# Performance work log

Measured on AMD Instinct MI355X. Metric: run time of the kernel, lower is better.

Reference implementation:

```python
import jax, jax.numpy as jnp
import numpy as np

B, N, T = 32, 128, 16          # batch, nb_nodes, total algorithm steps (1 no-hint + T-1 hinted)
FN, FE, FG, FH = 16, 8, 8, 16  # raw node/edge/graph/hint feature widths
H, DEC = 128, 64               # hidden_dim, decoder output width
MSG_STEPS = 3                  # msg_passing_steps
NEG = -1e9


def setup_inputs() -> dict:
    key = jax.random.key(0)
    ks = jax.random.split(key, 20)
    def nrm(k, shape, s=0.1):
        return jax.random.normal(k, shape, dtype=jnp.float32) * s
    return dict(
        node_inputs=nrm(ks[0], (B, N, FN), 1.0),
        edge_inputs=nrm(ks[1], (B, N, N, FE), 1.0),
        graph_inputs=nrm(ks[2], (B, FG), 1.0),
        hints_in=nrm(ks[3], (T - 1, B, N, FH), 1.0),
        adj=jax.random.randint(ks[4], (B, N, N), 0, 2).astype(jnp.int32),
        W_enc_n=nrm(ks[5], (FN, H)),
        W_enc_h=nrm(ks[6], (FH, H)),
        W_enc_e=nrm(ks[7], (FE, H)),
        W_enc_g=nrm(ks[8], (FG, H)),
        W_m1=nrm(ks[9], (2 * H, H)),
        W_m2=nrm(ks[10], (2 * H, H)),
        W_me=nrm(ks[11], (H, H)),
        W_mg=nrm(ks[12], (H, H)),
        W_o1=nrm(ks[13], (2 * H, H)),
        W_o2=nrm(ks[14], (H, H)),
        W_dec_n=nrm(ks[15], (H, DEC)),
        W_dec_e=nrm(ks[16], (H, DEC)),
    )


def reference(node_inputs, edge_inputs, graph_inputs, hints_in, adj,
              W_enc_n, W_enc_h, W_enc_e, W_enc_g,
              W_m1, W_m2, W_me, W_mg, W_o1, W_o2, W_dec_n, W_dec_e):
    adj_m = (adj > 0)[..., None]                      # [B,N,N,1] receiver i <- sender j
    # Encoder (edge/graph parts are step-invariant; hoisting is math-equivalent)
    edge_fts = edge_inputs @ W_enc_e                  # [B,N,N,H]
    graph_fts = graph_inputs @ W_enc_g                # [B,H]
    msg_e = edge_fts @ W_me                           # [B,N,N,H]
    msg_g = (graph_fts @ W_mg)[:, None, None, :]      # [B,1,1,H]
    base_node = node_inputs @ W_enc_n                 # [B,N,H]
    # Step 0 has no hint; steps 1..T-1 use hints_in[step-1]
    hints_all = jnp.concatenate(
        [jnp.zeros((1,) + hints_in.shape[1:], hints_in.dtype), hints_in], axis=0)

    def step(hidden, hint):
        node_fts = base_node + hint @ W_enc_h         # [B,N,H]
        edge_out = None
        for _ in range(MSG_STEPS):                    # PGN message passing
            z = jnp.concatenate([node_fts, hidden], axis=-1)   # [B,N,2H]
            msgs = jax.nn.relu((z @ W_m1)[:, :, None, :]
                               + (z @ W_m2)[:, None, :, :]
                               + msg_e + msg_g)       # [B,N,N,H]
            agg = jnp.where(adj_m, msgs, NEG).max(axis=2)      # max over senders j
            hidden = jax.nn.relu(z @ W_o1 + agg @ W_o2)        # [B,N,H]
            edge_out = msgs
        # Decoder: node head + masked-max-pooled edge head
        edge_agg = jnp.where(adj_m, edge_out, NEG).max(axis=2)
        out = hidden @ W_dec_n + edge_agg @ W_dec_e   # [B,N,DEC]
        return hidden, out

    hidden0 = jnp.zeros((node_inputs.shape[0], node_inputs.shape[1], H),
                        node_inputs.dtype)
    _, outs = jax.lax.scan(step, hidden0, hints_all)  # outs: [T,B,N,DEC]
    return outs
```

## Files before the change

### kernel.cpp

```cpp
#include <hip/hip_runtime.h>
#include <hip/hip_bf16.h>
#include <stdint.h>

#define BB 32
#define NN 128
#define TT 16
#define FN 16
#define FE 8
#define FG 8
#define FH 16
#define HH 128
#define DEC 64


__global__ __launch_bounds__(HH) void prep1(const float* __restrict__ node,
                                            const float* __restrict__ Wn,
                                            float* __restrict__ base_node) {
    int row = blockIdx.x;
    int h = threadIdx.x;
    float acc = 0.f;
#pragma unroll
    for (int f = 0; f < FN; ++f)
        acc += node[row * FN + f] * Wn[f * HH + h];
    base_node[row * HH + h] = acc;
}

__global__ __launch_bounds__(HH) void prep2(const float* __restrict__ graph,
                                            const float* __restrict__ Wg,
                                            const float* __restrict__ Wmg,
                                            const float* __restrict__ Wee,
                                            const float* __restrict__ Wme,
                                            float* __restrict__ mg,
                                            float* __restrict__ We) {
    int h = threadIdx.x;
    if (blockIdx.x < BB) {
        int b = blockIdx.x;
        __shared__ float gf[HH];
        float acc = 0.f;
#pragma unroll
        for (int f = 0; f < FG; ++f) acc += graph[b * FG + f] * Wg[f * HH + h];
        gf[h] = acc;
        __syncthreads();
        float a2 = 0.f;
#pragma unroll 16
        for (int k = 0; k < HH; ++k) a2 += gf[k] * Wmg[k * HH + h];
        mg[b * HH + h] = a2;
    } else {
        int f = blockIdx.x - BB;
        float acc = 0.f;
#pragma unroll 16
        for (int k = 0; k < HH; ++k) acc += Wee[f * HH + k] * Wme[k * HH + h];
        We[f * HH + h] = acc;
    }
}

__device__ __forceinline__ uint32_t bf16rne(float v) {
    uint32_t b = __float_as_uint(v);
    return (b + 0x7fffu + ((b >> 16) & 1u)) >> 16;
}

__global__ __launch_bounds__(HH) void prep3(const float* __restrict__ edge,
                                            const int* __restrict__ adj,
                                            uint4* __restrict__ eg16,
                                            int* __restrict__ jl,
                                            int* __restrict__ cnt) {
    int bi = blockIdx.x;
    int j = threadIdx.x;
    __shared__ int w0cnt, totc, j0s;
    bool valid = adj[(size_t)bi * NN + j] > 0;
    unsigned long long mask = __ballot(valid);
    int lane = j & 63;
    int wave = j >> 6;
    int prefix = __popcll(mask & ((1ull << lane) - 1ull));
    int wcount = __popcll(mask);
    if (wave == 0 && lane == 0) w0cnt = wcount;
    __syncthreads();
    int base = (wave == 1) ? w0cnt : 0;
    if (wave == 1 && lane == 0) totc = w0cnt + wcount;
    int pos = base + prefix;
    if (valid && pos == 0) j0s = j;
    __syncthreads();
    int c = totc;
    int cpad = (c + 7) & ~7;
    if (j == 0) cnt[bi] = cpad;

    if (valid) {
        jl[bi * NN + pos] = j;
        const float* src = edge + ((size_t)bi * NN + j) * FE;
        uint4 r;
        r.x = bf16rne(src[0]) | (bf16rne(src[1]) << 16);
        r.y = bf16rne(src[2]) | (bf16rne(src[3]) << 16);
        r.z = bf16rne(src[4]) | (bf16rne(src[5]) << 16);
        r.w = bf16rne(src[6]) | (bf16rne(src[7]) << 16);
        eg16[(size_t)bi * NN + pos] = r;
    }
    if (c > 0 && j >= c && j < cpad) {
        int j0 = j0s;
        jl[bi * NN + j] = j0;
        const float* src = edge + ((size_t)bi * NN + j0) * FE;
        uint4 r;
        r.x = bf16rne(src[0]) | (bf16rne(src[1]) << 16);
        r.y = bf16rne(src[2]) | (bf16rne(src[3]) << 16);
        r.z = bf16rne(src[4]) | (bf16rne(src[5]) << 16);
        r.w = bf16rne(src[6]) | (bf16rne(src[7]) << 16);
        eg16[(size_t)bi * NN + j] = r;
    }
}

__global__ __launch_bounds__(HH) void prepW(
    const float* __restrict__ Wh, const float* __restrict__ Wm1,
    const float* __restrict__ Wm2, const float* __restrict__ Wo1,
    float* __restrict__ WhW) {
    const int h = threadIdx.x;
    const int m = blockIdx.x >> 4;
    const int f = blockIdx.x & 15;
    const float* __restrict__ W = (m == 0) ? Wm1 : (m == 1) ? Wm2 : Wo1;
    float acc = 0.f;
#pragma unroll 16
    for (int k = 0; k < HH; ++k)
        acc = fmaf(Wh[f * HH + k], W[k * HH + h], acc);
    WhW[(m * FH + f) * HH + h] = acc;
}

__global__ __launch_bounds__(256) void prepI(
    const float* __restrict__ Wm1, const float* __restrict__ Wm2,
    const float* __restrict__ Wo1, float* __restrict__ Wi) {
    int idx = blockIdx.x * 256 + threadIdx.x;
    int kk = idx / 1536;
    int rem = idx - kk * 1536;
    int h = rem / 12;
    int q = rem - h * 12;
    int m = q >> 2;
    int u = q & 3;
    const float* __restrict__ W = (m == 0) ? Wm1 : (m == 1) ? Wm2 : Wo1;
    Wi[idx] = W[(HH + kk * 4 + u) * HH + h];
}

__global__ __launch_bounds__(512, 4) void prepB(
    const float* __restrict__ base_node,
    const float* __restrict__ Wm1, const float* __restrict__ Wm2,
    const float* __restrict__ Wo1, const float* __restrict__ mg,
    float* __restrict__ baseW) {
    __shared__ float zs[8][HH];
    const int tid = threadIdx.x;
    const int lane = tid & 127;
    const int grp = tid >> 7;
    const int bid = blockIdx.x;
    const int tile = (bid & 7) * 64 + (bid >> 3);
    const int row0 = tile * 8;
    const int rg0 = grp * 2, rg1 = rg0 + 1;

    zs[rg0][lane] = base_node[(size_t)(row0 + rg0) * HH + lane];
    zs[rg1][lane] = base_node[(size_t)(row0 + rg1) * HH + lane];
    __syncthreads();

    float acc[2][3];
#pragma unroll
    for (int e = 0; e < 2; ++e) { acc[e][0] = 0.f; acc[e][1] = 0.f; acc[e][2] = 0.f; }

#pragma unroll 4
    for (int kk = 0; kk < 32; ++kk) {
        const int k0 = kk * 4;
        float4 z0 = *(const float4*)&zs[rg0][k0];
        float4 z1 = *(const float4*)&zs[rg1][k0];
#define PBU(COMP, KO)                                                   \
        {                                                               \
            const float w1 = Wm1[(k0 + KO) * HH + lane];                \
            const float w2 = Wm2[(k0 + KO) * HH + lane];                \
            const float w3 = Wo1[(k0 + KO) * HH + lane];                \
            acc[0][0] = fmaf(z0.COMP, w1, acc[0][0]);                   \
            acc[1][0] = fmaf(z1.COMP, w1, acc[1][0]);                   \
            acc[0][1] = fmaf(z0.COMP, w2, acc[0][1]);                   \
            acc[1][1] = fmaf(z1.COMP, w2, acc[1][1]);                   \
            acc[0][2] = fmaf(z0.COMP, w3, acc[0][2]);                   \
            acc[1][2] = fmaf(z1.COMP, w3, acc[1][2]);                   \
        }
        PBU(x, 0) PBU(y, 1) PBU(z, 2) PBU(w, 3)
#undef PBU
    }

#pragma unroll
    for (int e = 0; e < 2; ++e) {
        const int row = row0 + grp * 2 + e;
        const float mgv = mg[(row >> 7) * HH + lane];
        baseW[((size_t)0 * 4096 + row) * HH + lane] = acc[e][0] + mgv;
        baseW[((size_t)1 * 4096 + row) * HH + lane] = acc[e][1];
        baseW[((size_t)2 * 4096 + row) * HH + lane] = acc[e][2];
    }
}

__global__ __launch_bounds__(256, 4) void k1_gemm(
    const float* __restrict__ hid, const float* __restrict__ Wi,
    const float* __restrict__ baseW, const float* __restrict__ WhW,
    const float* __restrict__ hints,
    float* __restrict__ m1n, float* __restrict__ m2n, float* __restrict__ o1n,
    int t) {
    __shared__ float zs[8][HH];
    const int tid = threadIdx.x;
    const int lane = tid & 127;
    const int grp = tid >> 7;
    const int g4 = grp * 4;
    const int bid = blockIdx.x;
    const int tile = (bid & 7) * 64 + (bid >> 3);
    const int row0 = tile * 8;

#pragma unroll
    for (int rr = 0; rr < 4; ++rr)
        zs[g4 + rr][lane] = hid[(size_t)(row0 + g4 + rr) * HH + lane];
    __syncthreads();

    float acc[4][3];
#pragma unroll
    for (int r = 0; r < 4; ++r) { acc[r][0] = 0.f; acc[r][1] = 0.f; acc[r][2] = 0.f; }

#pragma unroll 2
    for (int kk = 0; kk < 32; ++kk) {
        const float* __restrict__ wb = Wi + ((size_t)kk * HH + lane) * 12;
        float4 w1 = *(const float4*)(wb);
        float4 w2 = *(const float4*)(wb + 4);
        float4 w3 = *(const float4*)(wb + 8);
        float4 z0 = *(const float4*)&zs[g4 + 0][kk * 4];
        float4 z1 = *(const float4*)&zs[g4 + 1][kk * 4];
        float4 z2 = *(const float4*)&zs[g4 + 2][kk * 4];
        float4 z3 = *(const float4*)&zs[g4 + 3][kk * 4];
#define K1R(ZR, R)                                                      \
        acc[R][0] = fmaf(ZR.x, w1.x, acc[R][0]);                        \
        acc[R][0] = fmaf(ZR.y, w1.y, acc[R][0]);                        \
        acc[R][0] = fmaf(ZR.z, w1.z, acc[R][0]);                        \
        acc[R][0] = fmaf(ZR.w, w1.w, acc[R][0]);                        \
        acc[R][1] = fmaf(ZR.x, w2.x, acc[R][1]);                        \
        acc[R][1] = fmaf(ZR.y, w2.y, acc[R][1]);                        \
        acc[R][1] = fmaf(ZR.z, w2.z, acc[R][1]);                        \
        acc[R][1] = fmaf(ZR.w, w2.w, acc[R][1]);                        \
        acc[R][2] = fmaf(ZR.x, w3.x, acc[R][2]);                        \
        acc[R][2] = fmaf(ZR.y, w3.y, acc[R][2]);                        \
        acc[R][2] = fmaf(ZR.z, w3.z, acc[R][2]);                        \
        acc[R][2] = fmaf(ZR.w, w3.w, acc[R][2]);
        K1R(z0, 0) K1R(z1, 1) K1R(z2, 2) K1R(z3, 3)
#undef K1R
    }

#pragma unroll
    for (int e = 0; e < 4; ++e) {
        const int row = row0 + g4 + e;
        float s0 = baseW[((size_t)0 * 4096 + row) * HH + lane];
        float s1 = baseW[((size_t)1 * 4096 + row) * HH + lane];
        float s2 = baseW[((size_t)2 * 4096 + row) * HH + lane];
        if (t > 0) {
            const float* __restrict__ hr =
                hints + ((size_t)(t - 1) * BB * NN + row) * FH;
#pragma unroll
            for (int f = 0; f < FH; ++f) {
                const float hf = hr[f];
                s0 = fmaf(hf, WhW[(0 * FH + f) * HH + lane], s0);
                s1 = fmaf(hf, WhW[(1 * FH + f) * HH + lane], s1);
                s2 = fmaf(hf, WhW[(2 * FH + f) * HH + lane], s2);
            }
        }
        m1n[(size_t)row * HH + lane] = acc[e][0] + s0;
        m2n[(size_t)row * HH + lane] = acc[e][1] + s1;
        o1n[(size_t)row * HH + lane] = acc[e][2] + s2;
    }
}

__global__ __launch_bounds__(HH) void k2_max(
    const uint4* __restrict__ eg16, const int* __restrict__ jl,
    const int* __restrict__ cnt, const float* __restrict__ We,
    const float* __restrict__ m1p, const float* __restrict__ m2,
    const float* __restrict__ o1, const float* __restrict__ Wo2,
    const float* __restrict__ Wdn, const float* __restrict__ Wde,
    float* __restrict__ hid, float* __restrict__ out, int t, int last) {
    __shared__ float agg_lds[HH];
    __shared__ float hnew_lds[HH];
    const int h = threadIdx.x;
    const int bid = blockIdx.x;
    const int bi = (bid & 7) * 512 + (bid >> 3);
    const int b = bi >> 7;

    const float we0 = We[0 * HH + h], we1 = We[1 * HH + h];
    const float we2 = We[2 * HH + h], we3 = We[3 * HH + h];
    const float we4 = We[4 * HH + h], we5 = We[5 * HH + h];
    const float we6 = We[6 * HH + h], we7 = We[7 * HH + h];

    const uint4* __restrict__ egp = eg16 + (size_t)bi * NN;
    const int* __restrict__ jlb = jl + bi * NN;
    const float* __restrict__ m2b = m2 + (size_t)b * NN * HH;
    const int cp = cnt[bi];
    const float m1v = m1p[(size_t)bi * HH + h];
    const float o1v = o1[(size_t)bi * HH + h];

    float M = -3e38f;
    const int nch = cp >> 3;
    for (int ch = 0; ch < nch; ++ch) {
        const int k0 = ch * 8;
        uint4 raw[8];
        int jj[8];
        float mv[8];
#pragma unroll
        for (int s = 0; s < 8; ++s) raw[s] = egp[k0 + s];
#pragma unroll
        for (int s = 0; s < 8; ++s) jj[s] = jlb[k0 + s];
#pragma unroll
        for (int s = 0; s < 8; ++s) mv[s] = m2b[jj[s] * HH + h];
#pragma unroll
        for (int s = 0; s < 8; ++s) {
            uint32_t x = raw[s].x, y = raw[s].y, z = raw[s].z, w = raw[s].w;
            float e = __uint_as_float(x << 16) * we0;
            e = fmaf(__uint_as_float(x & 0xffff0000u), we1, e);
            e = fmaf(__uint_as_float(y << 16), we2, e);
            e = fmaf(__uint_as_float(y & 0xffff0000u), we3, e);
            e = fmaf(__uint_as_float(z << 16), we4, e);
            e = fmaf(__uint_as_float(z & 0xffff0000u), we5, e);
            e = fmaf(__uint_as_float(w << 16), we6, e);
            e = fmaf(__uint_as_float(w & 0xffff0000u), we7, e);
            M = fmaxf(M, e + mv[s]);
        }
    }
    float agg = (cp > 0) ? fmaxf(m1v + M, 0.f) : -1e9f;
    agg_lds[h] = agg;
    __syncthreads();

    float acc = o1v;
    const float4* a4 = (const float4*)agg_lds;
#pragma unroll 8
    for (int kk = 0; kk < 32; ++kk) {
        float4 a = a4[kk];
        acc = fmaf(a.x, Wo2[(kk * 4 + 0) * HH + h], acc);
        acc = fmaf(a.y, Wo2[(kk * 4 + 1) * HH + h], acc);
        acc = fmaf(a.z, Wo2[(kk * 4 + 2) * HH + h], acc);
        acc = fmaf(a.w, Wo2[(kk * 4 + 3) * HH + h], acc);
    }
    float hv = fmaxf(acc, 0.f);
    hid[(size_t)bi * HH + h] = hv;

    if (last) {
        hnew_lds[h] = hv;
        __syncthreads();
        if (h < DEC) {
            float a = 0.f, e2 = 0.f;
            const float4* h4p = (const float4*)hnew_lds;
#pragma unroll 8
            for (int kk = 0; kk < 32; ++kk) {
                float4 hv4 = h4p[kk];
                float4 av4 = a4[kk];
                a = fmaf(hv4.x, Wdn[(kk * 4 + 0) * DEC + h], a);
                a = fmaf(hv4.y, Wdn[(kk * 4 + 1) * DEC + h], a);
                a = fmaf(hv4.z, Wdn[(kk * 4 + 2) * DEC + h], a);
                a = fmaf(hv4.w, Wdn[(kk * 4 + 3) * DEC + h], a);
                e2 = fmaf(av4.x, Wde[(kk * 4 + 0) * DEC + h], e2);
                e2 = fmaf(av4.y, Wde[(kk * 4 + 1) * DEC + h], e2);
                e2 = fmaf(av4.z, Wde[(kk * 4 + 2) * DEC + h], e2);
                e2 = fmaf(av4.w, Wde[(kk * 4 + 3) * DEC + h], e2);
            }
            out[(((size_t)t * BB + b) * NN + (bi & 127)) * DEC + h] = a + e2;
        }
    }
}

extern "C" void kernel_launch(void* const* d_in, const int* in_sizes, int n_in,
                              void* d_out, int out_size, void* d_ws, size_t ws_size,
                              hipStream_t stream) {
    const float* node = (const float*)d_in[0];
    const float* edge = (const float*)d_in[1];
    const float* graph = (const float*)d_in[2];
    const float* hints = (const float*)d_in[3];
    const int* adj = (const int*)d_in[4];
    const float* Wn = (const float*)d_in[5];
    const float* Wh = (const float*)d_in[6];
    const float* Wee = (const float*)d_in[7];
    const float* Wg = (const float*)d_in[8];
    const float* Wm1 = (const float*)d_in[9];
    const float* Wm2 = (const float*)d_in[10];
    const float* Wme = (const float*)d_in[11];
    const float* Wmg = (const float*)d_in[12];
    const float* Wo1 = (const float*)d_in[13];
    const float* Wo2 = (const float*)d_in[14];
    const float* Wdn = (const float*)d_in[15];
    const float* Wde = (const float*)d_in[16];

    float* ws = (float*)d_ws;
    float* base_node = ws;
    float* We = ws + 524288;
    float* mg = ws + 525312;
    uint4* eg16 = (uint4*)(ws + 529408);
    int* jl = (int*)(ws + 2626560);
    int* cnt = (int*)(ws + 3150848);
    float* WhW = ws + 3154944;
    float* baseW = ws + 3161088;
    float* m1p = ws + 4733952;
    float* m2 = ws + 5258240;
    float* o1 = ws + 5782528;
    float* hid = ws + 6306816;
    float* Wi = ws + 6831104;
    float* out = (float*)d_out;

    const size_t MS = (size_t)4096 * HH;

    prep1<<<BB * NN, HH, 0, stream>>>(node, Wn, base_node);
    prep2<<<BB + FE, HH, 0, stream>>>(graph, Wg, Wmg, Wee, Wme, mg, We);
    prep3<<<BB * NN, HH, 0, stream>>>(edge, adj, eg16, jl, cnt);
    prepW<<<48, HH, 0, stream>>>(Wh, Wm1, Wm2, Wo1, WhW);
    prepI<<<192, 256, 0, stream>>>(Wm1, Wm2, Wo1, Wi);
    prepB<<<512, 512, 0, stream>>>(base_node, Wm1, Wm2, Wo1, mg, baseW);

    for (int r = 0; r < 48; ++r) {
        const int t = r / 3;
        const int last = ((r % 3) == 2) ? 1 : 0;
        const float *m1c, *m2c, *o1c;
        if (r == 0) {
            m1c = baseW; m2c = baseW + MS; o1c = baseW + 2 * MS;
        } else {
            k1_gemm<<<512, 256, 0, stream>>>(hid, Wi, baseW, WhW, hints,
                                             m1p, m2, o1, t);
            m1c = m1p; m2c = m2; o1c = o1;
        }
        k2_max<<<BB * NN, HH, 0, stream>>>(eg16, jl, cnt, We, m1c, m2c, o1c,
                                           Wo2, Wdn, Wde, hid, out, t, last);
    }
}
```

Before: 1.980 ms.

## Fuse per-round next-step GEMM into max-aggregation kernel with ping-pong buffers

Merges the projection GEMM (m1/m2/o1 for the next round) into the tail of the max-aggregation kernel, so each round launches one kernel instead of two. The new hidden state stays in shared memory rather than making a round trip through global memory. Outputs are double-buffered so the next round's projections do not overwrite data still being read by other blocks. Each block now handles 8 rows with 1024 threads, and it loses the 4-row register blocking of the old GEMM. That reduces reuse of the Wi weight loads and may lower occupancy.

```diff
diff --git a/kernel.cpp b/kernel.cpp
--- a/kernel.cpp
+++ b/kernel.cpp
@@ -189,92 +189,26 @@
     }
 }
 
-__global__ __launch_bounds__(256, 4) void k1_gemm(
-    const float* __restrict__ hid, const float* __restrict__ Wi,
-    const float* __restrict__ baseW, const float* __restrict__ WhW,
-    const float* __restrict__ hints,
+__global__ __launch_bounds__(1024, 2) void k12(
+    const uint4* __restrict__ eg16, const int* __restrict__ jl,
+    const int* __restrict__ cnt, const float* __restrict__ We,
+    const float* __restrict__ m1c, const float* __restrict__ m2c,
+    const float* __restrict__ o1c,
+    const float* __restrict__ Wi, const float* __restrict__ baseW,
+    const float* __restrict__ WhW, const float* __restrict__ hints,
+    const float* __restrict__ Wo2, const float* __restrict__ Wdn,
+    const float* __restrict__ Wde,
     float* __restrict__ m1n, float* __restrict__ m2n, float* __restrict__ o1n,
-    int t) {
-    __shared__ float zs[8][HH];
+    float* __restrict__ out, int t, int tnext, int last, int do_next) {
+    __shared__ float agg_lds[8][HH];
+    __shared__ float hv_lds[8][HH];
     const int tid = threadIdx.x;
-    const int lane = tid & 127;
-    const int grp = tid >> 7;
-    const int g4 = grp * 4;
     const int bid = blockIdx.x;
     const int tile = (bid & 7) * 64 + (bid >> 3);
-    const int row0 = tile * 8;
-
-#pragma unroll
-    for (int rr = 0; rr < 4; ++rr)
-        zs[g4 + rr][lane] = hid[(size_t)(row0 + g4 + rr) * HH + lane];
-    __syncthreads();
-
-    float acc[4][3];
-#pragma unroll
-    for (int r = 0; r < 4; ++r) { acc[r][0] = 0.f; acc[r][1] = 0.f; acc[r][2] = 0.f; }
-
-#pragma unroll 2
-    for (int kk = 0; kk < 32; ++kk) {
-        const float* __restrict__ wb = Wi + ((size_t)kk * HH + lane) * 12;
-        float4 w1 = *(const float4*)(wb);
-        float4 w2 = *(const float4*)(wb + 4);
-        float4 w3 = *(const float4*)(wb + 8);
-        float4 z0 = *(const float4*)&zs[g4 + 0][kk * 4];
-        float4 z1 = *(const float4*)&zs[g4 + 1][kk * 4];
-        float4 z2 = *(const float4*)&zs[g4 + 2][kk * 4];
-        float4 z3 = *(const float4*)&zs[g4 + 3][kk * 4];
-#define K1R(ZR, R)                                                      \
-        acc[R][0] = fmaf(ZR.x, w1.x, acc[R][0]);                        \
-        acc[R][0] = fmaf(ZR.y, w1.y, acc[R][0]);                        \
-        acc[R][0] = fmaf(ZR.z, w1.z, acc[R][0]);                        \
-        acc[R][0] = fmaf(ZR.w, w1.w, acc[R][0]);                        \
-        acc[R][1] = fmaf(ZR.x, w2.x, acc[R][1]);                        \
-        acc[R][1] = fmaf(ZR.y, w2.y, acc[R][1]);                        \
-        acc[R][1] = fmaf(ZR.z, w2.z, acc[R][1]);                        \
-        acc[R][1] = fmaf(ZR.w, w2.w, acc[R][1]);                        \
-        acc[R][2] = fmaf(ZR.x, w3.x, acc[R][2]);                        \
-        acc[R][2] = fmaf(ZR.y, w3.y, acc[R][2]);                        \
-        acc[R][2] = fmaf(ZR.z, w3.z, acc[R][2]);                        \
-        acc[R][2] = fmaf(ZR.w, w3.w, acc[R][2]);
-        K1R(z0, 0) K1R(z1, 1) K1R(z2, 2) K1R(z3, 3)
-#undef K1R
-    }
-
-#pragma unroll
-    for (int e = 0; e < 4; ++e) {
-        const int row = row0 + g4 + e;
-        float s0 = baseW[((size_t)0 * 4096 + row) * HH + lane];
-        float s1 = baseW[((size_t)1 * 4096 + row) * HH + lane];
-        float s2 = baseW[((size_t)2 * 4096 + row) * HH + lane];
-        if (t > 0) {
-            const float* __restrict__ hr =
-                hints + ((size_t)(t - 1) * BB * NN + row) * FH;
-#pragma unroll
-            for (int f = 0; f < FH; ++f) {
-                const float hf = hr[f];
-                s0 = fmaf(hf, WhW[(0 * FH + f) * HH + lane], s0);
-                s1 = fmaf(hf, WhW[(1 * FH + f) * HH + lane], s1);
-                s2 = fmaf(hf, WhW[(2 * FH + f) * HH + lane], s2);
-            }
-        }
-        m1n[(size_t)row * HH + lane] = acc[e][0] + s0;
-        m2n[(size_t)row * HH + lane] = acc[e][1] + s1;
-        o1n[(size_t)row * HH + lane] = acc[e][2] + s2;
-    }
-}
-
-__global__ __launch_bounds__(HH) void k2_max(
-    const uint4* __restrict__ eg16, const int* __restrict__ jl,
-    const int* __restrict__ cnt, const float* __restrict__ We,
-    const float* __restrict__ m1p, const float* __restrict__ m2,
-    const float* __restrict__ o1, const float* __restrict__ Wo2,
-    const float* __restrict__ Wdn, const float* __restrict__ Wde,
-    float* __restrict__ hid, float* __restrict__ out, int t, int last) {
-    __shared__ float agg_lds[HH];
-    __shared__ float hnew_lds[HH];
-    const int h = threadIdx.x;
-    const int bid = blockIdx.x;
-    const int bi = (bid & 7) * 512 + (bid >> 3);
+    const int bi0 = tile * 8;
+    const int il = tid >> 7;
+    const int h = tid & 127;
+    const int bi = bi0 + il;
     const int b = bi >> 7;
 
     const float we0 = We[0 * HH + h], we1 = We[1 * HH + h];
@@ -284,10 +218,10 @@
 
     const uint4* __restrict__ egp = eg16 + (size_t)bi * NN;
     const int* __restrict__ jlb = jl + bi * NN;
-    const float* __restrict__ m2b = m2 + (size_t)b * NN * HH;
+    const float* __restrict__ m2b = m2c + (size_t)b * NN * HH;
     const int cp = cnt[bi];
-    const float m1v = m1p[(size_t)bi * HH + h];
-    const float o1v = o1[(size_t)bi * HH + h];
+    const float m1v = m1c[(size_t)bi * HH + h];
+    const float o1v = o1c[(size_t)bi * HH + h];
 
     float M = -3e38f;
     const int nch = cp >> 3;
@@ -317,11 +251,11 @@
         }
     }
     float agg = (cp > 0) ? fmaxf(m1v + M, 0.f) : -1e9f;
-    agg_lds[h] = agg;
+    agg_lds[il][h] = agg;
     __syncthreads();
 
     float acc = o1v;
-    const float4* a4 = (const float4*)agg_lds;
+    const float4* a4 = (const float4*)&agg_lds[il][0];
 #pragma unroll 8
     for (int kk = 0; kk < 32; ++kk) {
         float4 a = a4[kk];
@@ -330,30 +264,72 @@
         acc = fmaf(a.z, Wo2[(kk * 4 + 2) * HH + h], acc);
         acc = fmaf(a.w, Wo2[(kk * 4 + 3) * HH + h], acc);
     }
-    float hv = fmaxf(acc, 0.f);
-    hid[(size_t)bi * HH + h] = hv;
-
-    if (last) {
-        hnew_lds[h] = hv;
-        __syncthreads();
-        if (h < DEC) {
-            float a = 0.f, e2 = 0.f;
-            const float4* h4p = (const float4*)hnew_lds;
+    hv_lds[il][h] = fmaxf(acc, 0.f);
+    __syncthreads();
+
+    if (last && tid < 512) {
+        const int dl = tid >> 6;
+        const int hh = tid & 63;
+        float a = 0.f, e2 = 0.f;
+        const float4* h4p = (const float4*)&hv_lds[dl][0];
+        const float4* ag4 = (const float4*)&agg_lds[dl][0];
 #pragma unroll 8
-            for (int kk = 0; kk < 32; ++kk) {
-                float4 hv4 = h4p[kk];
-                float4 av4 = a4[kk];
-                a = fmaf(hv4.x, Wdn[(kk * 4 + 0) * DEC + h], a);
-                a = fmaf(hv4.y, Wdn[(kk * 4 + 1) * DEC + h], a);
-                a = fmaf(hv4.z, Wdn[(kk * 4 + 2) * DEC + h], a);
-                a = fmaf(hv4.w, Wdn[(kk * 4 + 3) * DEC + h], a);
-                e2 = fmaf(av4.x, Wde[(kk * 4 + 0) * DEC + h], e2);
-                e2 = fmaf(av4.y, Wde[(kk * 4 + 1) * DEC + h], e2);
-                e2 = fmaf(av4.z, Wde[(kk * 4 + 2) * DEC + h], e2);
-                e2 = fmaf(av4.w, Wde[(kk * 4 + 3) * DEC + h], e2);
+        for (int kk = 0; kk < 32; ++kk) {
+            float4 hv4 = h4p[kk];
+            float4 av4 = ag4[kk];
+            a = fmaf(hv4.x, Wdn[(kk * 4 + 0) * DEC + hh], a);
+            a = fmaf(hv4.y, Wdn[(kk * 4 + 1) * DEC + hh], a);
+            a = fmaf(hv4.z, Wdn[(kk * 4 + 2) * DEC + hh], a);
+            a = fmaf(hv4.w, Wdn[(kk * 4 + 3) * DEC + hh], a);
+            e2 = fmaf(av4.x, Wde[(kk * 4 + 0) * DEC + hh], e2);
+            e2 = fmaf(av4.y, Wde[(kk * 4 + 1) * DEC + hh], e2);
+            e2 = fmaf(av4.z, Wde[(kk * 4 + 2) * DEC + hh], e2);
+            e2 = fmaf(av4.w, Wde[(kk * 4 + 3) * DEC + hh], e2);
+        }
+        const int bo = bi0 + dl;
+        out[(((size_t)t * BB + (bo >> 7)) * NN + (bo & 127)) * DEC + hh] = a + e2;
+    }
+
+    if (do_next) {
+        float a0 = 0.f, a1 = 0.f, a2 = 0.f;
+        const float4* zz = (const float4*)&hv_lds[il][0];
+#pragma unroll 4
+        for (int kk = 0; kk < 32; ++kk) {
+            const float* __restrict__ wb = Wi + ((size_t)kk * HH + h) * 12;
+            float4 w1 = *(const float4*)(wb);
+            float4 w2 = *(const float4*)(wb + 4);
+            float4 w3 = *(const float4*)(wb + 8);
+            float4 z = zz[kk];
+            a0 = fmaf(z.x, w1.x, a0);
+            a0 = fmaf(z.y, w1.y, a0);
+            a0 = fmaf(z.z, w1.z, a0);
+            a0 = fmaf(z.w, w1.w, a0);
+            a1 = fmaf(z.x, w2.x, a1);
+            a1 = fmaf(z.y, w2.y, a1);
+            a1 = fmaf(z.z, w2.z, a1);
+            a1 = fmaf(z.w, w2.w, a1);
+            a2 = fmaf(z.x, w3.x, a2);
+            a2 = fmaf(z.y, w3.y, a2);
+            a2 = fmaf(z.z, w3.z, a2);
+            a2 = fmaf(z.w, w3.w, a2);
+        }
+        float s0 = baseW[((size_t)0 * 4096 + bi) * HH + h];
+        float s1 = baseW[((size_t)1 * 4096 + bi) * HH + h];
+        float s2 = baseW[((size_t)2 * 4096 + bi) * HH + h];
+        if (tnext > 0) {
+            const float* __restrict__ hr =
+                hints + ((size_t)(tnext - 1) * BB * NN + bi) * FH;
+#pragma unroll
+            for (int f = 0; f < FH; ++f) {
+                const float hf = hr[f];
+                s0 = fmaf(hf, WhW[(0 * FH + f) * HH + h], s0);
+                s1 = fmaf(hf, WhW[(1 * FH + f) * HH + h], s1);
+                s2 = fmaf(hf, WhW[(2 * FH + f) * HH + h], s2);
             }
-            out[(((size_t)t * BB + b) * NN + (bi & 127)) * DEC + h] = a + e2;
-        }
+        }
+        m1n[(size_t)bi * HH + h] = a0 + s0;
+        m2n[(size_t)bi * HH + h] = a1 + s1;
+        o1n[(size_t)bi * HH + h] = a2 + s2;
     }
 }
 
@@ -387,11 +363,9 @@
     int* cnt = (int*)(ws + 3150848);
     float* WhW = ws + 3154944;
     float* baseW = ws + 3161088;
-    float* m1p = ws + 4733952;
-    float* m2 = ws + 5258240;
-    float* o1 = ws + 5782528;
-    float* hid = ws + 6306816;
-    float* Wi = ws + 6831104;
+    float* mA = ws + 4733952;
+    float* mB = ws + 6306816;
+    float* Wi = ws + 7879680;
     float* out = (float*)d_out;
 
     const size_t MS = (size_t)4096 * HH;
@@ -406,15 +380,21 @@
     for (int r = 0; r < 48; ++r) {
         const int t = r / 3;
         const int last = ((r % 3) == 2) ? 1 : 0;
+        const int tnext = t + last;
+        const int do_next = (r < 47) ? 1 : 0;
+
         const float *m1c, *m2c, *o1c;
         if (r == 0) {
             m1c = baseW; m2c = baseW + MS; o1c = baseW + 2 * MS;
         } else {
-            k1_gemm<<<512, 256, 0, stream>>>(hid, Wi, baseW, WhW, hints,
-                                             m1p, m2, o1, t);
-            m1c = m1p; m2c = m2; o1c = o1;
-        }
-        k2_max<<<BB * NN, HH, 0, stream>>>(eg16, jl, cnt, We, m1c, m2c, o1c,
-                                           Wo2, Wdn, Wde, hid, out, t, last);
-    }
-}
+            float* cb = ((r - 1) & 1) ? mB : mA;
+            m1c = cb; m2c = cb + MS; o1c = cb + 2 * MS;
+        }
+        float* nb = (r & 1) ? mB : mA;
+
+        k12<<<512, 1024, 0, stream>>>(eg16, jl, cnt, We, m1c, m2c, o1c,
+                                      Wi, baseW, WhW, hints, Wo2, Wdn, Wde,
+                                      nb, nb + MS, nb + 2 * MS,
+                                      out, t, tnext, last, do_next);
+    }
+}
```

After: 3.200 ms. +61.6%, slower.

## Precompute per-step hint projections and re-lay out recurrent weight tile

Applied to the files above, without the earlier changes.

Adds a prepH kernel that computes the step-invariant base plus hint-projection terms for all 16 steps once up front, storing them in a large zfull buffer. k1_gemm then just adds these precomputed terms instead of re-reading hints and WhW each launch. The Wi weight layout also changes so each lane's three float4 weight loads are contiguous across lanes, for better coalescing. The cost is an extra, fairly large workspace buffer (about 100 MB) and one more upfront kernel, and it drops the occupancy hint from k1_gemm's launch bounds.

```diff
diff --git a/kernel.cpp b/kernel.cpp
--- a/kernel.cpp
+++ b/kernel.cpp
@@ -122,18 +122,18 @@
     WhW[(m * FH + f) * HH + h] = acc;
 }
 
-__global__ __launch_bounds__(256) void prepI(
+__global__ __launch_bounds__(256) void prepJ(
     const float* __restrict__ Wm1, const float* __restrict__ Wm2,
-    const float* __restrict__ Wo1, float* __restrict__ Wi) {
+    const float* __restrict__ Wo1, float* __restrict__ Wj) {
     int idx = blockIdx.x * 256 + threadIdx.x;
     int kk = idx / 1536;
     int rem = idx - kk * 1536;
-    int h = rem / 12;
-    int q = rem - h * 12;
-    int m = q >> 2;
-    int u = q & 3;
+    int m = rem >> 9;
+    int r2 = rem & 511;
+    int h = r2 >> 2;
+    int u = r2 & 3;
     const float* __restrict__ W = (m == 0) ? Wm1 : (m == 1) ? Wm2 : Wo1;
-    Wi[idx] = W[(HH + kk * 4 + u) * HH + h];
+    Wj[idx] = W[(HH + kk * 4 + u) * HH + h];
 }
 
 __global__ __launch_bounds__(512, 4) void prepB(
@@ -189,12 +189,46 @@
     }
 }
 
-__global__ __launch_bounds__(256, 4) void k1_gemm(
-    const float* __restrict__ hid, const float* __restrict__ Wi,
+__global__ __launch_bounds__(256) void prepH(
     const float* __restrict__ baseW, const float* __restrict__ WhW,
-    const float* __restrict__ hints,
-    float* __restrict__ m1n, float* __restrict__ m2n, float* __restrict__ o1n,
-    int t) {
+    const float* __restrict__ hints, float* __restrict__ zfull) {
+    const int tid = threadIdx.x;
+    const int lane = tid & 127;
+    const int grp = tid >> 7;
+    const int bid = blockIdx.x;
+    const int t = bid >> 9;
+    const int bl = bid & 511;
+    const int tile = (bl & 7) * 64 + (bl >> 3);
+    const int row0 = tile * 8 + grp * 4;
+    const size_t zo = (size_t)t * 3 * 4096 * HH;
+
+#pragma unroll
+    for (int e = 0; e < 4; ++e) {
+        const int row = row0 + e;
+        float s0 = baseW[((size_t)0 * 4096 + row) * HH + lane];
+        float s1 = baseW[((size_t)1 * 4096 + row) * HH + lane];
+        float s2 = baseW[((size_t)2 * 4096 + row) * HH + lane];
+        if (t > 0) {
+            const float* __restrict__ hr =
+                hints + ((size_t)(t - 1) * BB * NN + row) * FH;
+#pragma unroll
+            for (int f = 0; f < FH; ++f) {
+                const float hf = hr[f];
+                s0 = fmaf(hf, WhW[(0 * FH + f) * HH + lane], s0);
+                s1 = fmaf(hf, WhW[(1 * FH + f) * HH + lane], s1);
+                s2 = fmaf(hf, WhW[(2 * FH + f) * HH + lane], s2);
+            }
+        }
+        zfull[zo + ((size_t)0 * 4096 + row) * HH + lane] = s0;
+        zfull[zo + ((size_t)1 * 4096 + row) * HH + lane] = s1;
+        zfull[zo + ((size_t)2 * 4096 + row) * HH + lane] = s2;
+    }
+}
+
+__global__ __launch_bounds__(256) void k1_gemm(
+    const float* __restrict__ hid, const float* __restrict__ Wj,
+    const float* __restrict__ zp,
+    float* __restrict__ m1n, float* __restrict__ m2n, float* __restrict__ o1n) {
     __shared__ float zs[8][HH];
     const int tid = threadIdx.x;
     const int lane = tid & 127;
@@ -215,10 +249,10 @@
 
 #pragma unroll 2
     for (int kk = 0; kk < 32; ++kk) {
-        const float* __restrict__ wb = Wi + ((size_t)kk * HH + lane) * 12;
+        const float* __restrict__ wb = Wj + (size_t)kk * 1536 + lane * 4;
         float4 w1 = *(const float4*)(wb);
-        float4 w2 = *(const float4*)(wb + 4);
-        float4 w3 = *(const float4*)(wb + 8);
+        float4 w2 = *(const float4*)(wb + 512);
+        float4 w3 = *(const float4*)(wb + 1024);
         float4 z0 = *(const float4*)&zs[g4 + 0][kk * 4];
         float4 z1 = *(const float4*)&zs[g4 + 1][kk * 4];
         float4 z2 = *(const float4*)&zs[g4 + 2][kk * 4];
@@ -243,23 +277,12 @@
 #pragma unroll
     for (int e = 0; e < 4; ++e) {
         const int row = row0 + g4 + e;
-        float s0 = baseW[((size_t)0 * 4096 + row) * HH + lane];
-        float s1 = baseW[((size_t)1 * 4096 + row) * HH + lane];
-        float s2 = baseW[((size_t)2 * 4096 + row) * HH + lane];
-        if (t > 0) {
-            const float* __restrict__ hr =
-                hints + ((size_t)(t - 1) * BB * NN + row) * FH;
-#pragma unroll
-            for (int f = 0; f < FH; ++f) {
-                const float hf = hr[f];
-                s0 = fmaf(hf, WhW[(0 * FH + f) * HH + lane], s0);
-                s1 = fmaf(hf, WhW[(1 * FH + f) * HH + lane], s1);
-                s2 = fmaf(hf, WhW[(2 * FH + f) * HH + lane], s2);
-            }
-        }
-        m1n[(size_t)row * HH + lane] = acc[e][0] + s0;
-        m2n[(size_t)row * HH + lane] = acc[e][1] + s1;
-        o1n[(size_t)row * HH + lane] = acc[e][2] + s2;
+        m1n[(size_t)row * HH + lane] =
+            acc[e][0] + zp[((size_t)0 * 4096 + row) * HH + lane];
+        m2n[(size_t)row * HH + lane] =
+            acc[e][1] + zp[((size_t)1 * 4096 + row) * HH + lane];
+        o1n[(size_t)row * HH + lane] =
+            acc[e][2] + zp[((size_t)2 * 4096 + row) * HH + lane];
     }
 }
 
@@ -391,7 +414,8 @@
     float* m2 = ws + 5258240;
     float* o1 = ws + 5782528;
     float* hid = ws + 6306816;
-    float* Wi = ws + 6831104;
+    float* Wj = ws + 6831104;
+    float* zfull = ws + 6880256;
     float* out = (float*)d_out;
 
     const size_t MS = (size_t)4096 * HH;
@@ -400,18 +424,19 @@
     prep2<<<BB + FE, HH, 0, stream>>>(graph, Wg, Wmg, Wee, Wme, mg, We);
     prep3<<<BB * NN, HH, 0, stream>>>(edge, adj, eg16, jl, cnt);
     prepW<<<48, HH, 0, stream>>>(Wh, Wm1, Wm2, Wo1, WhW);
-    prepI<<<192, 256, 0, stream>>>(Wm1, Wm2, Wo1, Wi);
+    prepJ<<<192, 256, 0, stream>>>(Wm1, Wm2, Wo1, Wj);
     prepB<<<512, 512, 0, stream>>>(base_node, Wm1, Wm2, Wo1, mg, baseW);
+    prepH<<<8192, 256, 0, stream>>>(baseW, WhW, hints, zfull);
 
     for (int r = 0; r < 48; ++r) {
         const int t = r / 3;
         const int last = ((r % 3) == 2) ? 1 : 0;
+        const float* zt = zfull + (size_t)t * 3 * MS;
         const float *m1c, *m2c, *o1c;
         if (r == 0) {
-            m1c = baseW; m2c = baseW + MS; o1c = baseW + 2 * MS;
+            m1c = zt; m2c = zt + MS; o1c = zt + 2 * MS;
         } else {
-            k1_gemm<<<512, 256, 0, stream>>>(hid, Wi, baseW, WhW, hints,
-                                             m1p, m2, o1, t);
+            k1_gemm<<<512, 256, 0, stream>>>(hid, Wj, zt, m1p, m2, o1);
             m1c = m1p; m2c = m2; o1c = o1;
         }
         k2_max<<<BB * NN, HH, 0, stream>>>(eg16, jl, cnt, We, m1c, m2c, o1c,
```

New measurement: 1.832 ms. 7.5% less time.
